# Kernel tuning notes

Measured on AMD Instinct MI355X. Metric: run time of the kernel, lower is better.

The kernel has to match this reference:

```python
import jax, jax.numpy as jnp
import numpy as np

B, N, E = 256, 4096, 65536  # graphs, nodes/graph (64*64), edges/graph


def setup_inputs() -> dict:
    key = jax.random.key(0)
    k = jax.random.split(key, 6)
    x = jax.random.normal(k[0], (B, N, 3), dtype=jnp.float32)
    src = jax.random.randint(k[1], (E,), 0, N, dtype=jnp.int32)
    dst = jax.random.randint(k[2], (E,), 0, N, dtype=jnp.int32)
    W1 = jax.random.normal(k[3], (3, 64), dtype=jnp.float32) * 0.3
    b1 = jnp.zeros((64,), dtype=jnp.float32)
    Wfc = jax.random.normal(k[4], (N * 64, 1), dtype=jnp.float32) * 0.002
    bfc = jnp.zeros((1,), dtype=jnp.float32)
    return {"x": x, "W1": W1, "b1": b1, "Wfc": Wfc, "bfc": bfc,
            "src": src, "dst": dst}


def reference(x, W1, b1, Wfc, bfc, src, dst):
    # DGL GraphConv, norm='both': h = relu(D_in^{-1/2} A D_out^{-1/2} x W + b)
    ones = jnp.ones((E,), dtype=x.dtype)
    deg_out = jax.ops.segment_sum(ones, src, num_segments=N)
    deg_in = jax.ops.segment_sum(ones, dst, num_segments=N)
    c_src = jax.lax.rsqrt(jnp.maximum(deg_out, 1.0))  # [N]
    c_dst = jax.lax.rsqrt(jnp.maximum(deg_in, 1.0))   # [N]
    # gather normalized source features, scatter-add into destinations
    msg = (x * c_src[None, :, None])[:, src]          # [B, E, 3]
    agg = jnp.zeros_like(x).at[:, dst].add(msg)       # [B, N, 3]
    h = jax.nn.relu((agg * c_dst[None, :, None]) @ W1 + b1)  # [B, N, 64]
    # fc: flatten per graph, Linear(N*64 -> 1) + sigmoid
    logits = h.reshape(x.shape[0], -1) @ Wfc + bfc    # [B, 1]
    return jax.nn.sigmoid(logits)
```

## Files before the change

### kernel.cpp

```cpp
#include <hip/hip_runtime.h>
#include <math.h>

#define Bg 256
#define Nn 4096
#define Ee 65536
#define Kk (Nn * 3)

__device__ __forceinline__ unsigned bf16r(float v) {
    unsigned b = __float_as_uint(v);
    return (b + 0x7fffu + ((b >> 16) & 1u)) >> 16;
}

__global__ __launch_bounds__(256) void k_prep(const int* __restrict__ src,
                                              const int* __restrict__ dst,
                                              int* __restrict__ deg_out,
                                              int* __restrict__ cursor,
                                              int* __restrict__ csr) {
    int e = blockIdx.x * 256 + threadIdx.x;
    if (e < Ee) {
        int s = src[e], d = dst[e];
        atomicAdd(&deg_out[s], 1);
        int ofs = atomicAdd(&cursor[d], 1) & 63;
        csr[(d << 6) + ofs] = s;
    }
}

__global__ __launch_bounds__(256) void k_transpose(const float* __restrict__ x,
                                                   const int* __restrict__ deg_out,
                                                   uint2* __restrict__ xsb) {
    __shared__ float4 tile4[64][49];
    __shared__ float cs[64];
    int t = threadIdx.x;
    int n0 = blockIdx.x * 64;
    int bq = blockIdx.y;
    if (t < 64) cs[t] = rsqrtf(fmaxf((float)deg_out[n0 + t], 1.0f));
    const float* xb = x + (size_t)bq * 64 * Kk + (size_t)n0 * 3;
#pragma unroll
    for (int i = 0; i < 12; i++) {
        int idx = i * 256 + t;
        int bi = idx / 48, j = idx - bi * 48;
        tile4[bi][j] = ((const float4*)(xb + (size_t)bi * Kk))[j];
    }
    __syncthreads();
    const float* tile = (const float*)tile4;
    uint2* outp = xsb + ((size_t)bq * Nn + n0) * 64;
#pragma unroll
    for (int i = 0; i < 16; i++) {
        int idx = i * 256 + t;
        int nn = idx >> 6, bl = idx & 63;
        float c = cs[nn];
        float f0 = tile[bl * 196 + nn * 3 + 0] * c;
        float f1 = tile[bl * 196 + nn * 3 + 1] * c;
        float f2 = tile[bl * 196 + nn * 3 + 2] * c;
        uint2 u;
        u.x = bf16r(f0) | (bf16r(f1) << 16);
        u.y = bf16r(f2);
        outp[(size_t)nn * 64 + bl] = u;
    }
}

__global__ __launch_bounds__(256) void k_main(const uint2* __restrict__ xsb,
                                              const float* __restrict__ W1,
                                              const float* __restrict__ b1,
                                              const float* __restrict__ Wfc,
                                              const int* __restrict__ cursor,
                                              const int* __restrict__ csr,
                                              float* __restrict__ partial) {
    __shared__ float4 sW14[64];
    __shared__ float sWfc[4][64];
    __shared__ float red[4][64];
    int t = threadIdx.x & 63;
    int w = threadIdx.x >> 6;
    int bq = blockIdx.x & 3;
    int g  = blockIdx.x >> 2;
    int n  = g * 4 + w;
    if (w == 0) sW14[t] = make_float4(W1[t], W1[64 + t], W1[128 + t], b1[t]);
    sWfc[w][t] = Wfc[n * 64 + t];
    __syncthreads();

    const uint2* slab = xsb + (size_t)bq * (Nn * 64);
    int myedge = csr[(n << 6) + t];
    int deg = cursor[n]; if (deg > 64) deg = 64;
    float a0 = 0.f, a1 = 0.f, a2 = 0.f;
    float c0 = 0.f, c1 = 0.f, c2 = 0.f;
    int i = 0;
    for (; i + 4 <= deg; i += 4) {
        int s0 = __shfl(myedge, i);
        int s1 = __shfl(myedge, i + 1);
        int s2 = __shfl(myedge, i + 2);
        int s3 = __shfl(myedge, i + 3);
        uint2 u0 = slab[(s0 << 6) + t];
        uint2 u1 = slab[(s1 << 6) + t];
        uint2 u2 = slab[(s2 << 6) + t];
        uint2 u3 = slab[(s3 << 6) + t];
        a0 += __uint_as_float(u0.x << 16); a1 += __uint_as_float(u0.x & 0xffff0000u); a2 += __uint_as_float(u0.y << 16);
        c0 += __uint_as_float(u1.x << 16); c1 += __uint_as_float(u1.x & 0xffff0000u); c2 += __uint_as_float(u1.y << 16);
        a0 += __uint_as_float(u2.x << 16); a1 += __uint_as_float(u2.x & 0xffff0000u); a2 += __uint_as_float(u2.y << 16);
        c0 += __uint_as_float(u3.x << 16); c1 += __uint_as_float(u3.x & 0xffff0000u); c2 += __uint_as_float(u3.y << 16);
    }
    for (; i < deg; i++) {
        int s = __shfl(myedge, i);
        uint2 u = slab[(s << 6) + t];
        a0 += __uint_as_float(u.x << 16);
        a1 += __uint_as_float(u.x & 0xffff0000u);
        a2 += __uint_as_float(u.y << 16);
    }
    a0 += c0; a1 += c1; a2 += c2;
    float cd = rsqrtf(fmaxf((float)deg, 1.0f));
    a0 *= cd; a1 *= cd; a2 *= cd;

    float part = 0.f;
#pragma unroll 8
    for (int f = 0; f < 64; f++) {
        float4 wv = sW14[f];
        float h = fmaf(a0, wv.x, fmaf(a1, wv.y, fmaf(a2, wv.z, wv.w)));
        part = fmaf(fmaxf(h, 0.f), sWfc[w][f], part);
    }
    red[w][t] = part;
    __syncthreads();
    if (w == 0) {
        float tot = (red[0][t] + red[1][t]) + (red[2][t] + red[3][t]);
        partial[(size_t)g * 256 + bq * 64 + t] = tot;
    }
}

__global__ __launch_bounds__(256) void k_reduce(const float* __restrict__ partial,
                                                float* __restrict__ out_acc) {
    int t = threadIdx.x;
    int g0 = blockIdx.x * 16;
    float s = 0.f;
#pragma unroll
    for (int g = 0; g < 16; g++) s += partial[(size_t)(g0 + g) * 256 + t];
    atomicAdd(&out_acc[t], s);
}

__global__ __launch_bounds__(256) void k_final(const float* __restrict__ out_acc,
                                               const float* __restrict__ bfc,
                                               float* __restrict__ out) {
    int t = threadIdx.x;
    float v = out_acc[t] + bfc[0];
    out[t] = 1.0f / (1.0f + expf(-v));
}

extern "C" void kernel_launch(void* const* d_in, const int* in_sizes, int n_in,
                              void* d_out, int out_size, void* d_ws, size_t ws_size,
                              hipStream_t stream) {
    const float* x   = (const float*)d_in[0];
    const float* W1  = (const float*)d_in[1];
    const float* b1  = (const float*)d_in[2];
    const float* Wfc = (const float*)d_in[3];
    const float* bfc = (const float*)d_in[4];
    const int*   src = (const int*)d_in[5];
    const int*   dst = (const int*)d_in[6];
    float* out = (float*)d_out;

    char* ws = (char*)d_ws;
    uint2* xsb = (uint2*)ws;
    const size_t Z = (size_t)4 * Nn * 64 * 8;
    int*   deg_out = (int*)(ws + Z);
    int*   cursor  = (int*)(ws + Z + 16384);
    float* out_acc = (float*)(ws + Z + 32768);
    int*   csr     = (int*)(ws + Z + 33792);
    float* partial = (float*)(ws + Z + 33792 + 1048576);

    hipMemsetAsync(ws + Z, 0, 33792, stream);
    k_prep<<<Ee / 256, 256, 0, stream>>>(src, dst, deg_out, cursor, csr);
    k_transpose<<<dim3(Nn / 64, 4), 256, 0, stream>>>(x, deg_out, xsb);
    k_main<<<1024 * 4, 256, 0, stream>>>(xsb, W1, b1, Wfc, cursor, csr, partial);
    k_reduce<<<64, 256, 0, stream>>>(partial, out_acc);
    k_final<<<1, 256, 0, stream>>>(out_acc, bfc, out);
}
```

Before: 110.0 us.

## Process four nodes per wave in k_main and merge reduce and final kernels

k_main now launches a quarter as many blocks, and each wave loops over four destination nodes. Edge indices come from uniform scalar loads of the CSR row instead of a per-lane load plus shuffle, and W1/b1/Wfc are read directly from global memory instead of being staged in LDS. The two-step reduce-then-sigmoid tail with a memset-cleared atomic accumulator becomes one 1024-thread block that reads all partials and applies the sigmoid. This cuts launch count and block overhead, at the cost of less parallelism per node and more serial work per wave.

```diff
diff --git a/kernel.cpp b/kernel.cpp
--- a/kernel.cpp
+++ b/kernel.cpp
@@ -66,80 +66,72 @@
                                               const int* __restrict__ cursor,
                                               const int* __restrict__ csr,
                                               float* __restrict__ partial) {
-    __shared__ float4 sW14[64];
-    __shared__ float sWfc[4][64];
     __shared__ float red[4][64];
-    int t = threadIdx.x & 63;
-    int w = threadIdx.x >> 6;
-    int bq = blockIdx.x & 3;
-    int g  = blockIdx.x >> 2;
-    int n  = g * 4 + w;
-    if (w == 0) sW14[t] = make_float4(W1[t], W1[64 + t], W1[128 + t], b1[t]);
-    sWfc[w][t] = Wfc[n * 64 + t];
-    __syncthreads();
-
-    const uint2* slab = xsb + (size_t)bq * (Nn * 64);
-    int myedge = csr[(n << 6) + t];
-    int deg = cursor[n]; if (deg > 64) deg = 64;
-    float a0 = 0.f, a1 = 0.f, a2 = 0.f;
-    float c0 = 0.f, c1 = 0.f, c2 = 0.f;
-    int i = 0;
-    for (; i + 4 <= deg; i += 4) {
-        int s0 = __shfl(myedge, i);
-        int s1 = __shfl(myedge, i + 1);
-        int s2 = __shfl(myedge, i + 2);
-        int s3 = __shfl(myedge, i + 3);
-        uint2 u0 = slab[(s0 << 6) + t];
-        uint2 u1 = slab[(s1 << 6) + t];
-        uint2 u2 = slab[(s2 << 6) + t];
-        uint2 u3 = slab[(s3 << 6) + t];
-        a0 += __uint_as_float(u0.x << 16); a1 += __uint_as_float(u0.x & 0xffff0000u); a2 += __uint_as_float(u0.y << 16);
-        c0 += __uint_as_float(u1.x << 16); c1 += __uint_as_float(u1.x & 0xffff0000u); c2 += __uint_as_float(u1.y << 16);
-        a0 += __uint_as_float(u2.x << 16); a1 += __uint_as_float(u2.x & 0xffff0000u); a2 += __uint_as_float(u2.y << 16);
-        c0 += __uint_as_float(u3.x << 16); c1 += __uint_as_float(u3.x & 0xffff0000u); c2 += __uint_as_float(u3.y << 16);
-    }
-    for (; i < deg; i++) {
-        int s = __shfl(myedge, i);
-        uint2 u = slab[(s << 6) + t];
-        a0 += __uint_as_float(u.x << 16);
-        a1 += __uint_as_float(u.x & 0xffff0000u);
-        a2 += __uint_as_float(u.y << 16);
-    }
-    a0 += c0; a1 += c1; a2 += c2;
-    float cd = rsqrtf(fmaxf((float)deg, 1.0f));
-    a0 *= cd; a1 *= cd; a2 *= cd;
-
+    const int t  = threadIdx.x & 63;
+    const int w  = threadIdx.x >> 6;
+    const int bq = blockIdx.x & 3;
+    const int g  = blockIdx.x >> 2;
+    const uint2* __restrict__ slab = xsb + (size_t)bq * (Nn * 64);
     float part = 0.f;
+#pragma unroll
+    for (int j = 0; j < 4; j++) {
+        const int n = (g << 4) + (w << 2) + j;
+        const int* __restrict__ crow = csr + (n << 6);
+        int deg = cursor[n]; if (deg > 64) deg = 64;
+        float a0 = 0.f, a1 = 0.f, a2 = 0.f;
+        float c0 = 0.f, c1 = 0.f, c2 = 0.f;
+        int i = 0;
+        for (; i + 4 <= deg; i += 4) {
+            int s0 = crow[i], s1 = crow[i + 1], s2 = crow[i + 2], s3 = crow[i + 3];
+            uint2 u0 = slab[(s0 << 6) + t];
+            uint2 u1 = slab[(s1 << 6) + t];
+            uint2 u2 = slab[(s2 << 6) + t];
+            uint2 u3 = slab[(s3 << 6) + t];
+            a0 += __uint_as_float(u0.x << 16); a1 += __uint_as_float(u0.x & 0xffff0000u); a2 += __uint_as_float(u0.y << 16);
+            c0 += __uint_as_float(u1.x << 16); c1 += __uint_as_float(u1.x & 0xffff0000u); c2 += __uint_as_float(u1.y << 16);
+            a0 += __uint_as_float(u2.x << 16); a1 += __uint_as_float(u2.x & 0xffff0000u); a2 += __uint_as_float(u2.y << 16);
+            c0 += __uint_as_float(u3.x << 16); c1 += __uint_as_float(u3.x & 0xffff0000u); c2 += __uint_as_float(u3.y << 16);
+        }
+        for (; i < deg; i++) {
+            int s = crow[i];
+            uint2 u = slab[(s << 6) + t];
+            a0 += __uint_as_float(u.x << 16);
+            a1 += __uint_as_float(u.x & 0xffff0000u);
+            a2 += __uint_as_float(u.y << 16);
+        }
+        a0 += c0; a1 += c1; a2 += c2;
+        const float cd = rsqrtf(fmaxf((float)deg, 1.0f));
+        a0 *= cd; a1 *= cd; a2 *= cd;
+        const float* __restrict__ wrow = Wfc + ((size_t)n << 6);
 #pragma unroll 8
-    for (int f = 0; f < 64; f++) {
-        float4 wv = sW14[f];
-        float h = fmaf(a0, wv.x, fmaf(a1, wv.y, fmaf(a2, wv.z, wv.w)));
-        part = fmaf(fmaxf(h, 0.f), sWfc[w][f], part);
+        for (int f = 0; f < 64; f++) {
+            float h = fmaf(a0, W1[f], fmaf(a1, W1[64 + f], fmaf(a2, W1[128 + f], b1[f])));
+            part = fmaf(fmaxf(h, 0.f), wrow[f], part);
+        }
     }
     red[w][t] = part;
     __syncthreads();
     if (w == 0) {
         float tot = (red[0][t] + red[1][t]) + (red[2][t] + red[3][t]);
-        partial[(size_t)g * 256 + bq * 64 + t] = tot;
+        partial[(g << 8) + (bq << 6) + t] = tot;
     }
 }
 
-__global__ __launch_bounds__(256) void k_reduce(const float* __restrict__ partial,
-                                                float* __restrict__ out_acc) {
-    int t = threadIdx.x;
-    int g0 = blockIdx.x * 16;
-    float s = 0.f;
-#pragma unroll
-    for (int g = 0; g < 16; g++) s += partial[(size_t)(g0 + g) * 256 + t];
-    atomicAdd(&out_acc[t], s);
-}
-
-__global__ __launch_bounds__(256) void k_final(const float* __restrict__ out_acc,
+__global__ __launch_bounds__(1024) void k_tail(const float* __restrict__ partial,
                                                const float* __restrict__ bfc,
                                                float* __restrict__ out) {
-    int t = threadIdx.x;
-    float v = out_acc[t] + bfc[0];
-    out[t] = 1.0f / (1.0f + expf(-v));
+    __shared__ float red[4][256];
+    int b = threadIdx.x & 255;
+    int q = threadIdx.x >> 8;
+    float s = 0.f;
+#pragma unroll 8
+    for (int g = q * 64; g < q * 64 + 64; g++) s += partial[(g << 8) + b];
+    red[q][b] = s;
+    __syncthreads();
+    if (q == 0) {
+        float v = (red[0][b] + red[1][b]) + (red[2][b] + red[3][b]) + bfc[0];
+        out[b] = 1.0f / (1.0f + expf(-v));
+    }
 }
 
 extern "C" void kernel_launch(void* const* d_in, const int* in_sizes, int n_in,
@@ -159,14 +151,12 @@
     const size_t Z = (size_t)4 * Nn * 64 * 8;
     int*   deg_out = (int*)(ws + Z);
     int*   cursor  = (int*)(ws + Z + 16384);
-    float* out_acc = (float*)(ws + Z + 32768);
-    int*   csr     = (int*)(ws + Z + 33792);
-    float* partial = (float*)(ws + Z + 33792 + 1048576);
+    int*   csr     = (int*)(ws + Z + 32768);
+    float* partial = (float*)(ws + Z + 32768 + 1048576);
 
-    hipMemsetAsync(ws + Z, 0, 33792, stream);
+    hipMemsetAsync(ws + Z, 0, 32768, stream);
     k_prep<<<Ee / 256, 256, 0, stream>>>(src, dst, deg_out, cursor, csr);
     k_transpose<<<dim3(Nn / 64, 4), 256, 0, stream>>>(x, deg_out, xsb);
-    k_main<<<1024 * 4, 256, 0, stream>>>(xsb, W1, b1, Wfc, cursor, csr, partial);
-    k_reduce<<<64, 256, 0, stream>>>(partial, out_acc);
-    k_final<<<1, 256, 0, stream>>>(out_acc, bfc, out);
+    k_main<<<1024, 256, 0, stream>>>(xsb, W1, b1, Wfc, cursor, csr, partial);
+    k_tail<<<1, 1024, 0, stream>>>(partial, bfc, out);
 }
```

Result: slower. 117.8 us (+7.1%).

## Fuse prep with transpose and fold reduce/final into main kernel

Applied to the files above, without the earlier changes.

Combines the edge-CSR build and the x transpose into one launch by moving the source-degree normalization out of the transpose and into the gather loop, where each lane computes its edge's rsqrt scale and broadcasts it by shuffle. The reduce and sigmoid kernels are removed: main-kernel blocks atomically accumulate into the output accumulator, and the last block, found with a done counter, applies the sigmoid. This removes three launches and the partial buffer, at the cost of extra shuffles and FMAs in the inner loop and contended atomics on 256 addresses.

```diff
diff --git a/kernel.cpp b/kernel.cpp
--- a/kernel.cpp
+++ b/kernel.cpp
@@ -11,29 +11,27 @@
     return (b + 0x7fffu + ((b >> 16) & 1u)) >> 16;
 }
 
-__global__ __launch_bounds__(256) void k_prep(const int* __restrict__ src,
-                                              const int* __restrict__ dst,
-                                              int* __restrict__ deg_out,
-                                              int* __restrict__ cursor,
-                                              int* __restrict__ csr) {
-    int e = blockIdx.x * 256 + threadIdx.x;
-    if (e < Ee) {
+__global__ __launch_bounds__(256) void k_pt(const float* __restrict__ x,
+                                            const int* __restrict__ src,
+                                            const int* __restrict__ dst,
+                                            int* __restrict__ deg_out,
+                                            int* __restrict__ cursor,
+                                            int* __restrict__ csr,
+                                            uint2* __restrict__ xsb) {
+    __shared__ float4 tile4[64][49];
+    const int t = threadIdx.x;
+    const int bid = blockIdx.x;
+    if (bid < 256) {
+        int e = bid * 256 + t;
         int s = src[e], d = dst[e];
         atomicAdd(&deg_out[s], 1);
         int ofs = atomicAdd(&cursor[d], 1) & 63;
         csr[(d << 6) + ofs] = s;
+        return;
     }
-}
-
-__global__ __launch_bounds__(256) void k_transpose(const float* __restrict__ x,
-                                                   const int* __restrict__ deg_out,
-                                                   uint2* __restrict__ xsb) {
-    __shared__ float4 tile4[64][49];
-    __shared__ float cs[64];
-    int t = threadIdx.x;
-    int n0 = blockIdx.x * 64;
-    int bq = blockIdx.y;
-    if (t < 64) cs[t] = rsqrtf(fmaxf((float)deg_out[n0 + t], 1.0f));
+    const int bt = bid - 256;
+    const int ni = bt & 63, bq = bt >> 6;
+    const int n0 = ni * 64;
     const float* xb = x + (size_t)bq * 64 * Kk + (size_t)n0 * 3;
 #pragma unroll
     for (int i = 0; i < 12; i++) {
@@ -48,10 +46,9 @@
     for (int i = 0; i < 16; i++) {
         int idx = i * 256 + t;
         int nn = idx >> 6, bl = idx & 63;
-        float c = cs[nn];
-        float f0 = tile[bl * 196 + nn * 3 + 0] * c;
-        float f1 = tile[bl * 196 + nn * 3 + 1] * c;
-        float f2 = tile[bl * 196 + nn * 3 + 2] * c;
+        float f0 = tile[bl * 196 + nn * 3 + 0];
+        float f1 = tile[bl * 196 + nn * 3 + 1];
+        float f2 = tile[bl * 196 + nn * 3 + 2];
         uint2 u;
         u.x = bf16r(f0) | (bf16r(f1) << 16);
         u.y = bf16r(f2);
@@ -63,47 +60,66 @@
                                               const float* __restrict__ W1,
                                               const float* __restrict__ b1,
                                               const float* __restrict__ Wfc,
+                                              const float* __restrict__ bfc,
+                                              const int* __restrict__ deg_out,
                                               const int* __restrict__ cursor,
                                               const int* __restrict__ csr,
-                                              float* __restrict__ partial) {
+                                              float* __restrict__ out_acc,
+                                              int* __restrict__ done,
+                                              float* __restrict__ out) {
     __shared__ float4 sW14[64];
     __shared__ float sWfc[4][64];
     __shared__ float red[4][64];
-    int t = threadIdx.x & 63;
-    int w = threadIdx.x >> 6;
-    int bq = blockIdx.x & 3;
-    int g  = blockIdx.x >> 2;
-    int n  = g * 4 + w;
+    __shared__ int lastblk;
+    const int t = threadIdx.x & 63;
+    const int w = threadIdx.x >> 6;
+    const int bq = blockIdx.x & 3;
+    const int g  = blockIdx.x >> 2;
+    const int n  = g * 4 + w;
     if (w == 0) sW14[t] = make_float4(W1[t], W1[64 + t], W1[128 + t], b1[t]);
     sWfc[w][t] = Wfc[n * 64 + t];
     __syncthreads();
 
-    const uint2* slab = xsb + (size_t)bq * (Nn * 64);
-    int myedge = csr[(n << 6) + t];
+    const uint2* __restrict__ slab = xsb + (size_t)bq * (Nn * 64);
+    int e = csr[(n << 6) + t] & (Nn - 1);
+    float cs_t = rsqrtf(fmaxf((float)deg_out[e], 1.0f));
     int deg = cursor[n]; if (deg > 64) deg = 64;
     float a0 = 0.f, a1 = 0.f, a2 = 0.f;
     float c0 = 0.f, c1 = 0.f, c2 = 0.f;
     int i = 0;
     for (; i + 4 <= deg; i += 4) {
-        int s0 = __shfl(myedge, i);
-        int s1 = __shfl(myedge, i + 1);
-        int s2 = __shfl(myedge, i + 2);
-        int s3 = __shfl(myedge, i + 3);
+        int s0 = __shfl(e, i);
+        int s1 = __shfl(e, i + 1);
+        int s2 = __shfl(e, i + 2);
+        int s3 = __shfl(e, i + 3);
+        float q0 = __shfl(cs_t, i);
+        float q1 = __shfl(cs_t, i + 1);
+        float q2 = __shfl(cs_t, i + 2);
+        float q3 = __shfl(cs_t, i + 3);
         uint2 u0 = slab[(s0 << 6) + t];
         uint2 u1 = slab[(s1 << 6) + t];
         uint2 u2 = slab[(s2 << 6) + t];
         uint2 u3 = slab[(s3 << 6) + t];
-        a0 += __uint_as_float(u0.x << 16); a1 += __uint_as_float(u0.x & 0xffff0000u); a2 += __uint_as_float(u0.y << 16);
-        c0 += __uint_as_float(u1.x << 16); c1 += __uint_as_float(u1.x & 0xffff0000u); c2 += __uint_as_float(u1.y << 16);
-        a0 += __uint_as_float(u2.x << 16); a1 += __uint_as_float(u2.x & 0xffff0000u); a2 += __uint_as_float(u2.y << 16);
-        c0 += __uint_as_float(u3.x << 16); c1 += __uint_as_float(u3.x & 0xffff0000u); c2 += __uint_as_float(u3.y << 16);
+        a0 = fmaf(q0, __uint_as_float(u0.x << 16), a0);
+        a1 = fmaf(q0, __uint_as_float(u0.x & 0xffff0000u), a1);
+        a2 = fmaf(q0, __uint_as_float(u0.y << 16), a2);
+        c0 = fmaf(q1, __uint_as_float(u1.x << 16), c0);
+        c1 = fmaf(q1, __uint_as_float(u1.x & 0xffff0000u), c1);
+        c2 = fmaf(q1, __uint_as_float(u1.y << 16), c2);
+        a0 = fmaf(q2, __uint_as_float(u2.x << 16), a0);
+        a1 = fmaf(q2, __uint_as_float(u2.x & 0xffff0000u), a1);
+        a2 = fmaf(q2, __uint_as_float(u2.y << 16), a2);
+        c0 = fmaf(q3, __uint_as_float(u3.x << 16), c0);
+        c1 = fmaf(q3, __uint_as_float(u3.x & 0xffff0000u), c1);
+        c2 = fmaf(q3, __uint_as_float(u3.y << 16), c2);
     }
     for (; i < deg; i++) {
-        int s = __shfl(myedge, i);
+        int s = __shfl(e, i);
+        float q = __shfl(cs_t, i);
         uint2 u = slab[(s << 6) + t];
-        a0 += __uint_as_float(u.x << 16);
-        a1 += __uint_as_float(u.x & 0xffff0000u);
-        a2 += __uint_as_float(u.y << 16);
+        a0 = fmaf(q, __uint_as_float(u.x << 16), a0);
+        a1 = fmaf(q, __uint_as_float(u.x & 0xffff0000u), a1);
+        a2 = fmaf(q, __uint_as_float(u.y << 16), a2);
     }
     a0 += c0; a1 += c1; a2 += c2;
     float cd = rsqrtf(fmaxf((float)deg, 1.0f));
@@ -120,26 +136,16 @@
     __syncthreads();
     if (w == 0) {
         float tot = (red[0][t] + red[1][t]) + (red[2][t] + red[3][t]);
-        partial[(size_t)g * 256 + bq * 64 + t] = tot;
+        atomicAdd(&out_acc[(bq << 6) + t], tot);
     }
-}
-
-__global__ __launch_bounds__(256) void k_reduce(const float* __restrict__ partial,
-                                                float* __restrict__ out_acc) {
-    int t = threadIdx.x;
-    int g0 = blockIdx.x * 16;
-    float s = 0.f;
-#pragma unroll
-    for (int g = 0; g < 16; g++) s += partial[(size_t)(g0 + g) * 256 + t];
-    atomicAdd(&out_acc[t], s);
-}
-
-__global__ __launch_bounds__(256) void k_final(const float* __restrict__ out_acc,
-                                               const float* __restrict__ bfc,
-                                               float* __restrict__ out) {
-    int t = threadIdx.x;
-    float v = out_acc[t] + bfc[0];
-    out[t] = 1.0f / (1.0f + expf(-v));
+    __threadfence();
+    __syncthreads();
+    if (threadIdx.x == 0) lastblk = (atomicAdd(done, 1) == (int)gridDim.x - 1);
+    __syncthreads();
+    if (lastblk) {
+        float v = atomicAdd(&out_acc[threadIdx.x], 0.0f) + bfc[0];
+        out[threadIdx.x] = 1.0f / (1.0f + expf(-v));
+    }
 }
 
 extern "C" void kernel_launch(void* const* d_in, const int* in_sizes, int n_in,
@@ -160,13 +166,11 @@
     int*   deg_out = (int*)(ws + Z);
     int*   cursor  = (int*)(ws + Z + 16384);
     float* out_acc = (float*)(ws + Z + 32768);
-    int*   csr     = (int*)(ws + Z + 33792);
-    float* partial = (float*)(ws + Z + 33792 + 1048576);
+    int*   done    = (int*)(ws + Z + 33792);
+    int*   csr     = (int*)(ws + Z + 34048);
 
-    hipMemsetAsync(ws + Z, 0, 33792, stream);
-    k_prep<<<Ee / 256, 256, 0, stream>>>(src, dst, deg_out, cursor, csr);
-    k_transpose<<<dim3(Nn / 64, 4), 256, 0, stream>>>(x, deg_out, xsb);
-    k_main<<<1024 * 4, 256, 0, stream>>>(xsb, W1, b1, Wfc, cursor, csr, partial);
-    k_reduce<<<64, 256, 0, stream>>>(partial, out_acc);
-    k_final<<<1, 256, 0, stream>>>(out_acc, bfc, out);
+    hipMemsetAsync(ws + Z, 0, 34048, stream);
+    k_pt<<<512, 256, 0, stream>>>(x, src, dst, deg_out, cursor, csr, xsb);
+    k_main<<<1024 * 4, 256, 0, stream>>>(xsb, W1, b1, Wfc, bfc, deg_out, cursor, csr,
+                                         out_acc, done, out);
 }
```

Result: slower. 345.2 us (+214.0%).
